# Optimization experiments

Measured on AMD Instinct MI355X. Metric: run time of the kernel, lower is better.

## Reference

```python
import jax, jax.numpy as jnp
import numpy as np

N, E = 50000, 800000
IN_DIM, HID, HEADS, OUT_DIM = 128, 64, 4, 40
NEG_SLOPE = 0.2


def setup_inputs() -> dict:
    key = jax.random.key(0)
    ks = jax.random.split(key, 12)
    x = jax.random.normal(ks[0], (N, IN_DIM), dtype=jnp.float32)
    edge_index = jax.random.randint(ks[1], (2, E), 0, N, dtype=jnp.int64)
    timesteps = jax.random.randint(ks[2], (N,), 0, 100, dtype=jnp.int64)
    s = 1.0 / np.sqrt(IN_DIM)
    W_proj = jax.random.uniform(ks[3], (IN_DIM, HID), jnp.float32, -s, s)
    b_proj = jnp.zeros((HID,), jnp.float32)
    time_emb = jax.random.normal(ks[4], (100, HID), dtype=jnp.float32)
    sg = 1.0 / np.sqrt(HID)
    W_gat = jax.random.uniform(ks[5], (HID, HEADS * HID), jnp.float32, -sg, sg)
    att_src = jax.random.uniform(ks[6], (HEADS, HID), jnp.float32, -sg, sg)
    att_dst = jax.random.uniform(ks[7], (HEADS, HID), jnp.float32, -sg, sg)
    b_gat = jnp.zeros((HEADS * HID,), jnp.float32)
    sc = 1.0 / np.sqrt(HEADS * HID)
    W_cls = jax.random.uniform(ks[8], (HEADS * HID, OUT_DIM), jnp.float32, -sc, sc)
    b_cls = jnp.zeros((OUT_DIM,), jnp.float32)
    return {"x": x, "edge_index": edge_index, "timesteps": timesteps,
            "W_proj": W_proj, "b_proj": b_proj, "time_emb": time_emb,
            "W_gat": W_gat, "att_src": att_src, "att_dst": att_dst, "b_gat": b_gat,
            "W_cls": W_cls, "b_cls": b_cls}


def reference(x, edge_index, timesteps, W_proj, b_proj, time_emb,
              W_gat, att_src, att_dst, b_gat, W_cls, b_cls):
    n = x.shape[0]
    # feature projection + ReLU + time embedding
    h0 = jax.nn.relu(x @ W_proj + b_proj) + time_emb[timesteps]  # [N, HID]
    # --- GATConv (PyG semantics, add_self_loops=True, concat heads) ---
    h = (h0 @ W_gat).reshape(n, HEADS, HID)              # [N, H, C]
    a_src = jnp.einsum('nhc,hc->nh', h, att_src)         # [N, H]
    a_dst = jnp.einsum('nhc,hc->nh', h, att_dst)
    loops = jnp.arange(n, dtype=edge_index.dtype)
    src = jnp.concatenate([edge_index[0], loops])        # [E+N]
    dst = jnp.concatenate([edge_index[1], loops])
    e = jax.nn.leaky_relu(a_src[src] + a_dst[dst], NEG_SLOPE)  # [E+N, H]
    # segment softmax over incoming edges per destination node
    m = jax.ops.segment_max(e, dst, num_segments=n)      # [N, H]
    p = jnp.exp(e - m[dst])
    denom = jax.ops.segment_sum(p, dst, num_segments=n)  # [N, H]
    alpha = p / (denom[dst] + 1e-16)                     # [E+N, H]
    msg = alpha[:, :, None] * h[src]                     # [E+N, H, C]
    agg = jax.ops.segment_sum(msg, dst, num_segments=n)  # [N, H, C]
    gat_out = agg.reshape(n, HEADS * HID) + b_gat
    # ReLU + (dropout is identity in eval) + classifier
    return jax.nn.relu(gat_out) @ W_cls + b_cls          # [N, OUT_DIM]
```

## Files before the change

kernel.cpp:

```cpp
#include <hip/hip_runtime.h>
#include <hip/hip_fp16.h>

#define IN_DIM 128
#define HID 64
#define HEADS 4
#define OUT_DIM 40
#define CAP 64
#define NEG 0.2f
#define PA_EPB 4096
#define BKT_SH 9
#define BKT_CAP 10240
#define GPAD 264

__device__ __forceinline__ float lrelu(float v) { return v > 0.f ? v : NEG * v; }

union HU { float2 f2; __half2 h2[2]; };
union HU2 { float4 f4; __half2 h2[4]; };

typedef _Float16 h2v __attribute__((ext_vector_type(2)));
union DU { float4 f4; h2v h[4]; };

typedef _Float16 f16x8 __attribute__((ext_vector_type(8)));
typedef float f32x4 __attribute__((ext_vector_type(4)));
union FU { float4 f4; f16x8 v; };

__device__ __forceinline__ float4 unpack_h4(float2 bits) {
    HU u; u.f2 = bits;
    float2 lo = __half22float2(u.h2[0]);
    float2 hi = __half22float2(u.h2[1]);
    return make_float4(lo.x, lo.y, hi.x, hi.y);
}

__global__ __launch_bounds__(256) void partA_kernel(
    const int* __restrict__ ei, int E, int nbkt, int paBlocks,
    int* __restrict__ cnt, unsigned int* __restrict__ ebuf,
    const float* __restrict__ Wg, const float* __restrict__ attS,
    const float* __restrict__ attD, const float* __restrict__ Wc,
    float* __restrict__ aSf, float* __restrict__ aDf,
    __half* __restrict__ WgT, __half* __restrict__ WcTg)
{
    if (blockIdx.x >= paBlocks) {
        int gid = (blockIdx.x - paBlocks) * 256 + threadIdx.x;
        if (gid < 256) {
            int k = gid >> 2, hd = gid & 3;
            const float* wr = Wg + k * 256 + hd * 64;
            const float* as = attS + hd * 64;
            const float* ad = attD + hd * 64;
            float ss = 0.f, dd = 0.f;
            for (int c = 0; c < 64; ++c) { float w = wr[c]; ss += w * as[c]; dd += w * ad[c]; }
            aSf[k * 4 + hd] = ss;
            aDf[k * 4 + hd] = dd;
        } else if (gid < 256 + 256 * HID) {
            int i = gid - 256;
            int o = i >> 6, k = i & 63;
            WgT[i] = __float2half(Wg[k * 256 + o]);
        } else if (gid < 256 + 256 * HID + OUT_DIM * 256) {
            int i = gid - 256 - 256 * HID;
            int o = i >> 8, k = i & 255;
            WcTg[i] = __float2half(Wc[k * OUT_DIM + o]);
        }
        return;
    }

    __shared__ int localCnt[128];
    __shared__ int baseArr[128];
    for (int i = threadIdx.x; i < nbkt; i += 256) localCnt[i] = 0;
    __syncthreads();

    const int e0 = blockIdx.x * PA_EPB + threadIdx.x;
    unsigned short l[16];
#pragma unroll
    for (int j = 0; j < 16; ++j) {
        int e = e0 + j * 256;
        if (e < E) {
            int d = ei[E + e];
            l[j] = (unsigned short)atomicAdd(&localCnt[d >> BKT_SH], 1);
        }
    }
    __syncthreads();
    for (int i = threadIdx.x; i < nbkt; i += 256)
        baseArr[i] = atomicAdd(&cnt[i], localCnt[i]);
    __syncthreads();
#pragma unroll
    for (int j = 0; j < 16; ++j) {
        int e = e0 + j * 256;
        if (e < E) {
            int s = ei[e];
            int d = ei[E + e];
            int b = d >> BKT_SH;
            int off = baseArr[b] + (int)l[j];
            if (off < BKT_CAP)
                ebuf[(size_t)b * BKT_CAP + off] =
                    ((unsigned)(d & ((1 << BKT_SH) - 1)) << 16) | (unsigned)s;
        }
    }
}

__global__ __launch_bounds__(256) void partB_kernel(
    const unsigned int* __restrict__ ebuf, const int* __restrict__ cnt,
    int* __restrict__ deg, unsigned short* __restrict__ csr, int N)
{
    __shared__ int cntL[512];
    __shared__ unsigned short rows[512 * CAP];
    const int b = blockIdx.x;
    for (int i = threadIdx.x; i < 512; i += 256) cntL[i] = 0;
    __syncthreads();

    int cb = cnt[b]; cb = cb < BKT_CAP ? cb : BKT_CAP;
    const unsigned int* eb = ebuf + (size_t)b * BKT_CAP;
    for (int i = threadIdx.x; i < cb; i += 256) {
        unsigned v = eb[i];
        int dloc = v >> 16;
        int slot = atomicAdd(&cntL[dloc], 1);
        if (slot < CAP) rows[dloc * CAP + slot] = (unsigned short)(v & 0xFFFFu);
    }
    __syncthreads();

    const int d0 = b << BKT_SH;
    for (int i = threadIdx.x; i < 512; i += 256) {
        int d = d0 + i;
        if (d < N) deg[d] = cntL[i];
    }
    int limRows = N - d0; limRows = limRows < 512 ? limRows : 512;
    if (limRows <= 0) return;
    const uint4* rsrc = (const uint4*)rows;
    uint4* rdst = (uint4*)(csr + (size_t)d0 * CAP);
    int nvec = (limRows * CAP) >> 3;
    for (int i = threadIdx.x; i < nvec; i += 256)
        rdst[i] = rsrc[i];
}

__global__ __launch_bounds__(256) void proj_kernel(
    const float* __restrict__ x, const float* __restrict__ Wp,
    const float* __restrict__ bp, const float* __restrict__ temb,
    const int* __restrict__ ts, const float* __restrict__ aSf,
    const float* __restrict__ aDf,
    __half* __restrict__ h0h, float* __restrict__ aS, float* __restrict__ aD, int N)
{
    __shared__ __half Wl[IN_DIM * HID];
    for (int i = threadIdx.x * 8; i < IN_DIM * HID; i += 256 * 8) {
        float4 wa = *(const float4*)(Wp + i);
        float4 wb = *(const float4*)(Wp + i + 4);
        HU2 u;
        u.h2[0] = __floats2half2_rn(wa.x, wa.y);
        u.h2[1] = __floats2half2_rn(wa.z, wa.w);
        u.h2[2] = __floats2half2_rn(wb.x, wb.y);
        u.h2[3] = __floats2half2_rn(wb.z, wb.w);
        *(float4*)(Wl + i) = u.f4;
    }
    __syncthreads();

    const int t = threadIdx.x;
    const int lane = t & 63, wq = t >> 6;
    const int cg = lane & 15, ng = lane >> 4;
    const int c0 = cg * 4;
    const int nodeBase = blockIdx.x * 32 + wq * 8 + ng * 2;

    float4 acc[2];
#pragma unroll
    for (int j = 0; j < 2; ++j) acc[j] = make_float4(0.f, 0.f, 0.f, 0.f);

    for (int k0 = 0; k0 < IN_DIM; k0 += 4) {
        float4 xv[2];
#pragma unroll
        for (int j = 0; j < 2; ++j) {
            int n = nodeBase + j; n = n < N ? n : N - 1;
            xv[j] = *(const float4*)(x + (size_t)n * IN_DIM + k0);
        }
        float4 wv[4];
#pragma unroll
        for (int kk = 0; kk < 4; ++kk)
            wv[kk] = unpack_h4(*(const float2*)(Wl + (k0 + kk) * HID + c0));
#pragma unroll
        for (int j = 0; j < 2; ++j) {
            const float* xs = (const float*)&xv[j];
#pragma unroll
            for (int kk = 0; kk < 4; ++kk) {
                acc[j].x += xs[kk] * wv[kk].x;
                acc[j].y += xs[kk] * wv[kk].y;
                acc[j].z += xs[kk] * wv[kk].z;
                acc[j].w += xs[kk] * wv[kk].w;
            }
        }
    }
    const float4 bb = *(const float4*)(bp + c0);
    float4 s0 = *(const float4*)(aSf + (c0 + 0) * 4);
    float4 s1 = *(const float4*)(aSf + (c0 + 1) * 4);
    float4 s2 = *(const float4*)(aSf + (c0 + 2) * 4);
    float4 s3 = *(const float4*)(aSf + (c0 + 3) * 4);
    float4 d0 = *(const float4*)(aDf + (c0 + 0) * 4);
    float4 d1 = *(const float4*)(aDf + (c0 + 1) * 4);
    float4 d2 = *(const float4*)(aDf + (c0 + 2) * 4);
    float4 d3 = *(const float4*)(aDf + (c0 + 3) * 4);
#pragma unroll
    for (int j = 0; j < 2; ++j) {
        int n = nodeBase + j;
        float4 r = make_float4(0.f, 0.f, 0.f, 0.f);
        if (n < N) {
            int tv = ts[n];
            float4 te = *(const float4*)(temb + (size_t)tv * HID + c0);
            r.x = fmaxf(acc[j].x + bb.x, 0.f) + te.x;
            r.y = fmaxf(acc[j].y + bb.y, 0.f) + te.y;
            r.z = fmaxf(acc[j].z + bb.z, 0.f) + te.z;
            r.w = fmaxf(acc[j].w + bb.w, 0.f) + te.w;
            HU u;
            u.h2[0] = __floats2half2_rn(r.x, r.y);
            u.h2[1] = __floats2half2_rn(r.z, r.w);
            *(float2*)(h0h + (size_t)n * HID + c0) = u.f2;
        }
        float4 pS, pD;
        pS.x = r.x * s0.x + r.y * s1.x + r.z * s2.x + r.w * s3.x;
        pS.y = r.x * s0.y + r.y * s1.y + r.z * s2.y + r.w * s3.y;
        pS.z = r.x * s0.z + r.y * s1.z + r.z * s2.z + r.w * s3.z;
        pS.w = r.x * s0.w + r.y * s1.w + r.z * s2.w + r.w * s3.w;
        pD.x = r.x * d0.x + r.y * d1.x + r.z * d2.x + r.w * d3.x;
        pD.y = r.x * d0.y + r.y * d1.y + r.z * d2.y + r.w * d3.y;
        pD.z = r.x * d0.z + r.y * d1.z + r.z * d2.z + r.w * d3.z;
        pD.w = r.x * d0.w + r.y * d1.w + r.z * d2.w + r.w * d3.w;
#pragma unroll
        for (int off = 8; off > 0; off >>= 1) {
            pS.x += __shfl_down(pS.x, off); pS.y += __shfl_down(pS.y, off);
            pS.z += __shfl_down(pS.z, off); pS.w += __shfl_down(pS.w, off);
            pD.x += __shfl_down(pD.x, off); pD.y += __shfl_down(pD.y, off);
            pD.z += __shfl_down(pD.z, off); pD.w += __shfl_down(pD.w, off);
        }
        if (cg == 0 && n < N) {
            *(float4*)(aS + (size_t)n * 4) = pS;
            *(float4*)(aD + (size_t)n * 4) = pD;
        }
    }
}

__global__ __launch_bounds__(256) void agg_kernel(
    const __half* __restrict__ h0h, const float* __restrict__ aS,
    const float* __restrict__ aD, const int* __restrict__ deg,
    const unsigned short* __restrict__ csr, __half* __restrict__ agg0h, int N)
{
    __shared__ float p_lds[4 * CAP * HEADS];
    __shared__ int   s_lds[4 * CAP];

    const int t = threadIdx.x;
    const int lane = t & 63, wq = t >> 6;
    const int n = blockIdx.x * 4 + wq;
    if (n >= N) return;
    const int hd16 = lane >> 4, li = lane & 15;

    const float adn = aD[n * 4 + hd16];
    const float es = lrelu(aS[n * 4 + hd16] + adn);

    int dn = deg[n]; dn = dn < CAP ? dn : CAP;
    const unsigned short* cs = csr + (size_t)n * CAP;
    float* pL = p_lds + wq * CAP * HEADS;
    int*   sL = s_lds + wq * CAP;

    float m = -1e30f;
    for (int i = li; i < dn; i += 16) {
        int src = cs[i];
        if (hd16 == 0) sL[i] = src << 7;
        float e = lrelu(aS[src * 4 + hd16] + adn);
        pL[i * HEADS + hd16] = e;
        m = fmaxf(m, e);
    }
#pragma unroll
    for (int off = 8; off > 0; off >>= 1)
        m = fmaxf(m, __shfl_xor(m, off));
    m = fmaxf(m, es);
    float mh[4], esh[4];
#pragma unroll
    for (int h = 0; h < 4; ++h) {
        mh[h]  = __shfl(m, h * 16);
        esh[h] = __shfl(es, h * 16);
    }

    float sp = 0.f;
    for (int idx = lane; idx < dn * 4; idx += 64) {
        float p = __expf(pL[idx] - mh[idx & 3]);
        pL[idx] = p;
        sp += p;
    }
#pragma unroll
    for (int off = 4; off < 64; off <<= 1)
        sp += __shfl_xor(sp, off);
    float pselfh[4], invh[4];
#pragma unroll
    for (int h = 0; h < 4; ++h) {
        float sh = __shfl(sp, h);
        pselfh[h] = __expf(esh[h] - mh[h]);
        invh[h] = 1.f / (sh + pselfh[h] + 1e-16f);
    }

    const int half = lane >> 5;
    const int ch2 = lane & 31;
    const char* hb = (const char*)h0h;
    const int laneByte = ch2 << 2;

    float2 acc[4];
    {
        float lo = 0.f, hi = 0.f;
        if (half == 0) {
            __half2 v2 = *(const __half2*)(hb + ((size_t)n << 7) + laneByte);
            float2 f = __half22float2(v2);
            lo = f.x; hi = f.y;
        }
#pragma unroll
        for (int h = 0; h < 4; ++h) {
            acc[h].x = pselfh[h] * lo;
            acc[h].y = pselfh[h] * hi;
        }
    }
    int i = 0;
    for (; i + 8 <= dn; i += 8) {
        int off0 = sL[i + 0 + half];
        int off1 = sL[i + 2 + half];
        int off2 = sL[i + 4 + half];
        int off3 = sL[i + 6 + half];
        __half2 v0 = *(const __half2*)(hb + off0 + laneByte);
        __half2 v1 = *(const __half2*)(hb + off1 + laneByte);
        __half2 v2 = *(const __half2*)(hb + off2 + laneByte);
        __half2 v3 = *(const __half2*)(hb + off3 + laneByte);
        float4 p0 = *(const float4*)(pL + (i + 0 + half) * 4);
        float4 p1 = *(const float4*)(pL + (i + 2 + half) * 4);
        float4 p2 = *(const float4*)(pL + (i + 4 + half) * 4);
        float4 p3 = *(const float4*)(pL + (i + 6 + half) * 4);
        float2 f;
        f = __half22float2(v0);
        acc[0].x += p0.x * f.x; acc[0].y += p0.x * f.y;
        acc[1].x += p0.y * f.x; acc[1].y += p0.y * f.y;
        acc[2].x += p0.z * f.x; acc[2].y += p0.z * f.y;
        acc[3].x += p0.w * f.x; acc[3].y += p0.w * f.y;
        f = __half22float2(v1);
        acc[0].x += p1.x * f.x; acc[0].y += p1.x * f.y;
        acc[1].x += p1.y * f.x; acc[1].y += p1.y * f.y;
        acc[2].x += p1.z * f.x; acc[2].y += p1.z * f.y;
        acc[3].x += p1.w * f.x; acc[3].y += p1.w * f.y;
        f = __half22float2(v2);
        acc[0].x += p2.x * f.x; acc[0].y += p2.x * f.y;
        acc[1].x += p2.y * f.x; acc[1].y += p2.y * f.y;
        acc[2].x += p2.z * f.x; acc[2].y += p2.z * f.y;
        acc[3].x += p2.w * f.x; acc[3].y += p2.w * f.y;
        f = __half22float2(v3);
        acc[0].x += p3.x * f.x; acc[0].y += p3.x * f.y;
        acc[1].x += p3.y * f.x; acc[1].y += p3.y * f.y;
        acc[2].x += p3.z * f.x; acc[2].y += p3.z * f.y;
        acc[3].x += p3.w * f.x; acc[3].y += p3.w * f.y;
    }
    for (; i + 2 <= dn; i += 2) {
        int off0 = sL[i + half];
        __half2 v0 = *(const __half2*)(hb + off0 + laneByte);
        float4 p0 = *(const float4*)(pL + (i + half) * 4);
        float2 f = __half22float2(v0);
        acc[0].x += p0.x * f.x; acc[0].y += p0.x * f.y;
        acc[1].x += p0.y * f.x; acc[1].y += p0.y * f.y;
        acc[2].x += p0.z * f.x; acc[2].y += p0.z * f.y;
        acc[3].x += p0.w * f.x; acc[3].y += p0.w * f.y;
    }
    if (i < dn && half == 0) {
        int off0 = sL[i];
        __half2 v0 = *(const __half2*)(hb + off0 + laneByte);
        float4 p0 = *(const float4*)(pL + i * 4);
        float2 f = __half22float2(v0);
        acc[0].x += p0.x * f.x; acc[0].y += p0.x * f.y;
        acc[1].x += p0.y * f.x; acc[1].y += p0.y * f.y;
        acc[2].x += p0.z * f.x; acc[2].y += p0.z * f.y;
        acc[3].x += p0.w * f.x; acc[3].y += p0.w * f.y;
    }
#pragma unroll
    for (int h = 0; h < 4; ++h) {
        acc[h].x += __shfl_xor(acc[h].x, 32);
        acc[h].y += __shfl_xor(acc[h].y, 32);
    }
    if (lane < 32) {
        __half2* dst = (__half2*)(agg0h + (size_t)n * 256);
#pragma unroll
        for (int h = 0; h < 4; ++h)
            dst[h * 32 + ch2] = __floats2half2_rn(acc[h].x * invh[h],
                                                  acc[h].y * invh[h]);
    }
}

__global__ __launch_bounds__(256) void gatcls_kernel(
    const __half* __restrict__ agg0h, const __half* __restrict__ WgT,
    const float* __restrict__ bg, const __half* __restrict__ WcTg,
    const float* __restrict__ bc, float* __restrict__ out, int N)
{
    __shared__ __half gtile[32 * GPAD];

    const int t = threadIdx.x;
    const int lane = t & 63, wq = t >> 6;
    const int m16 = lane & 15, quad = lane >> 4;
    const int nodeBase = blockIdx.x * 32;

    {
        const int h = wq;
        f32x4 acc[2][4];
#pragma unroll
        for (int mt = 0; mt < 2; ++mt)
#pragma unroll
            for (int nt = 0; nt < 4; ++nt)
                acc[mt][nt] = (f32x4){0.f, 0.f, 0.f, 0.f};

#pragma unroll
        for (int ks = 0; ks < 2; ++ks) {
            FU a[2], b[4];
#pragma unroll
            for (int mt = 0; mt < 2; ++mt) {
                int n = nodeBase + mt * 16 + m16; n = n < N ? n : N - 1;
                a[mt].f4 = *(const float4*)(agg0h + (size_t)n * 256 + h * 64 + ks * 32 + quad * 8);
            }
#pragma unroll
            for (int nt = 0; nt < 4; ++nt) {
                int o = h * 64 + nt * 16 + m16;
                b[nt].f4 = *(const float4*)(WgT + o * 64 + ks * 32 + quad * 8);
            }
#pragma unroll
            for (int mt = 0; mt < 2; ++mt)
#pragma unroll
                for (int nt = 0; nt < 4; ++nt)
                    acc[mt][nt] = __builtin_amdgcn_mfma_f32_16x16x32_f16(
                        a[mt].v, b[nt].v, acc[mt][nt], 0, 0, 0);
        }
#pragma unroll
        for (int nt = 0; nt < 4; ++nt) {
            int o = h * 64 + nt * 16 + m16;
            float bv = bg[o];
#pragma unroll
            for (int mt = 0; mt < 2; ++mt) {
#pragma unroll
                for (int r = 0; r < 4; ++r) {
                    int nloc = mt * 16 + quad * 4 + r;
                    gtile[nloc * GPAD + o] = __float2half(fmaxf(acc[mt][nt][r] + bv, 0.f));
                }
            }
        }
    }
    __syncthreads();

    {
        const int mt = wq >> 1;
        const int ntCount = (wq & 1) ? 1 : 2;
        const int ntBase = (wq & 1) ? 2 : 0;
        f32x4 acc2[2];
        acc2[0] = (f32x4){0.f, 0.f, 0.f, 0.f};
        acc2[1] = (f32x4){0.f, 0.f, 0.f, 0.f};
#pragma unroll
        for (int ks = 0; ks < 8; ++ks) {
            FU a; a.f4 = *(const float4*)(gtile + (mt * 16 + m16) * GPAD + ks * 32 + quad * 8);
            for (int q = 0; q < ntCount; ++q) {
                int o = (ntBase + q) * 16 + m16;
                int oc = o < OUT_DIM ? o : OUT_DIM - 1;
                FU b; b.f4 = *(const float4*)(WcTg + oc * 256 + ks * 32 + quad * 8);
                acc2[q] = __builtin_amdgcn_mfma_f32_16x16x32_f16(a.v, b.v, acc2[q], 0, 0, 0);
            }
        }
        for (int q = 0; q < ntCount; ++q) {
            int o = (ntBase + q) * 16 + m16;
            if (o < OUT_DIM) {
                float bv = bc[o];
#pragma unroll
                for (int r = 0; r < 4; ++r) {
                    int n = nodeBase + mt * 16 + quad * 4 + r;
                    if (n < N) out[(size_t)n * OUT_DIM + o] = acc2[q][r] + bv;
                }
            }
        }
    }
}

extern "C" void kernel_launch(void* const* d_in, const int* in_sizes, int n_in,
                              void* d_out, int out_size, void* d_ws, size_t ws_size,
                              hipStream_t stream) {
    const float* x    = (const float*)d_in[0];
    const int*   ei   = (const int*)d_in[1];
    const int*   ts   = (const int*)d_in[2];
    const float* Wp   = (const float*)d_in[3];
    const float* bp   = (const float*)d_in[4];
    const float* temb = (const float*)d_in[5];
    const float* Wg   = (const float*)d_in[6];
    const float* attS = (const float*)d_in[7];
    const float* attD = (const float*)d_in[8];
    const float* bg   = (const float*)d_in[9];
    const float* Wc   = (const float*)d_in[10];
    const float* bc   = (const float*)d_in[11];
    float* out = (float*)d_out;

    const int N = in_sizes[0] / IN_DIM;
    const int E = in_sizes[1] / 2;
    const int nbkt = (N + (1 << BKT_SH) - 1) >> BKT_SH;

    char* w = (char*)d_ws;
    __half*         h0h   = (__half*)w;         w += (size_t)N * HID * 2;
    __half*         agg0h = (__half*)w;         w += (size_t)N * 256 * 2;
    float*          aS    = (float*)w;          w += (size_t)N * HEADS * 4;
    float*          aD    = (float*)w;          w += (size_t)N * HEADS * 4;
    int*            deg   = (int*)w;            w += (size_t)N * 4;
    unsigned short* csr   = (unsigned short*)w; w += (size_t)N * CAP * 2;
    unsigned int*   ebuf  = (unsigned int*)w;   w += (size_t)nbkt * BKT_CAP * 4;
    int*            cnt   = (int*)w;            w += (size_t)nbkt * 4;
    float*          aSf   = (float*)w;          w += 256 * 4;
    float*          aDf   = (float*)w;          w += 256 * 4;
    __half*         WgT   = (__half*)w;         w += (size_t)256 * HID * 2;
    __half*         WcTg  = (__half*)w;         w += (size_t)OUT_DIM * 256 * 2;

    const int paBlocks = (E + PA_EPB - 1) / PA_EPB;
    const int prepWork = 256 + 256 * HID + OUT_DIM * 256;
    const int prepBlocks = (prepWork + 255) / 256;

    hipMemsetAsync(cnt, 0, (size_t)nbkt * 4, stream);
    partA_kernel<<<paBlocks + prepBlocks, 256, 0, stream>>>(
        ei, E, nbkt, paBlocks, cnt, ebuf, Wg, attS, attD, Wc, aSf, aDf, WgT, WcTg);
    partB_kernel<<<nbkt, 256, 0, stream>>>(ebuf, cnt, deg, csr, N);
    proj_kernel<<<(N + 31) / 32, 256, 0, stream>>>(x, Wp, bp, temb, ts, aSf, aDf,
                                                   h0h, aS, aD, N);
    agg_kernel<<<(N + 3) / 4, 256, 0, stream>>>(h0h, aS, aD, deg, csr, agg0h, N);
    gatcls_kernel<<<(N + 31) / 32, 256, 0, stream>>>(agg0h, WgT, bg, WcTg, bc, out, N);
}
```

Baseline: 211.2 us.

## Use fp16 dot2 projection with pre-packed weights and smaller edge buckets

The projection kernel now converts x to half2 pairs and accumulates with fdot2 against a k-pair-packed fp16 weight table. That table is built once in the partA prep blocks, which removes the per-block shared-memory staging of Wp and its barrier. The edge bucketing is also halved (256-node buckets, 2048 edges per partition block), so partB uses half the LDS, gets more blocks and has better occupancy. The trade-off is extra fp16 rounding of the x inputs, and many more buckets feeding the global count atomics.

```diff
diff --git a/kernel.cpp b/kernel.cpp
--- a/kernel.cpp
+++ b/kernel.cpp
@@ -7,9 +7,9 @@
 #define OUT_DIM 40
 #define CAP 64
 #define NEG 0.2f
-#define PA_EPB 4096
-#define BKT_SH 9
-#define BKT_CAP 10240
+#define PA_EPB 2048
+#define BKT_SH 8
+#define BKT_CAP 5120
 #define GPAD 264
 
 __device__ __forceinline__ float lrelu(float v) { return v > 0.f ? v : NEG * v; }
@@ -19,6 +19,7 @@
 
 typedef _Float16 h2v __attribute__((ext_vector_type(2)));
 union DU { float4 f4; h2v h[4]; };
+union H2U { __half2 h2; h2v v; };
 
 typedef _Float16 f16x8 __attribute__((ext_vector_type(8)));
 typedef float f32x4 __attribute__((ext_vector_type(4)));
@@ -36,8 +37,10 @@
     int* __restrict__ cnt, unsigned int* __restrict__ ebuf,
     const float* __restrict__ Wg, const float* __restrict__ attS,
     const float* __restrict__ attD, const float* __restrict__ Wc,
+    const float* __restrict__ Wp,
     float* __restrict__ aSf, float* __restrict__ aDf,
-    __half* __restrict__ WgT, __half* __restrict__ WcTg)
+    __half* __restrict__ WgT, __half* __restrict__ WcTg,
+    __half2* __restrict__ Wpp)
 {
     if (blockIdx.x >= paBlocks) {
         int gid = (blockIdx.x - paBlocks) * 256 + threadIdx.x;
@@ -58,19 +61,23 @@
             int i = gid - 256 - 256 * HID;
             int o = i >> 8, k = i & 255;
             WcTg[i] = __float2half(Wc[k * OUT_DIM + o]);
+        } else if (gid < 256 + 256 * HID + OUT_DIM * 256 + 64 * 64) {
+            int i = gid - 256 - 256 * HID - OUT_DIM * 256;
+            int kp = i >> 6, c = i & 63;
+            Wpp[i] = __floats2half2_rn(Wp[(2 * kp) * HID + c], Wp[(2 * kp + 1) * HID + c]);
         }
         return;
     }
 
-    __shared__ int localCnt[128];
-    __shared__ int baseArr[128];
+    __shared__ int localCnt[256];
+    __shared__ int baseArr[256];
     for (int i = threadIdx.x; i < nbkt; i += 256) localCnt[i] = 0;
     __syncthreads();
 
     const int e0 = blockIdx.x * PA_EPB + threadIdx.x;
-    unsigned short l[16];
-#pragma unroll
-    for (int j = 0; j < 16; ++j) {
+    unsigned short l[8];
+#pragma unroll
+    for (int j = 0; j < 8; ++j) {
         int e = e0 + j * 256;
         if (e < E) {
             int d = ei[E + e];
@@ -82,7 +89,7 @@
         baseArr[i] = atomicAdd(&cnt[i], localCnt[i]);
     __syncthreads();
 #pragma unroll
-    for (int j = 0; j < 16; ++j) {
+    for (int j = 0; j < 8; ++j) {
         int e = e0 + j * 256;
         if (e < E) {
             int s = ei[e];
@@ -100,10 +107,10 @@
     const unsigned int* __restrict__ ebuf, const int* __restrict__ cnt,
     int* __restrict__ deg, unsigned short* __restrict__ csr, int N)
 {
-    __shared__ int cntL[512];
-    __shared__ unsigned short rows[512 * CAP];
+    __shared__ int cntL[256];
+    __shared__ unsigned short rows[256 * CAP];
     const int b = blockIdx.x;
-    for (int i = threadIdx.x; i < 512; i += 256) cntL[i] = 0;
+    for (int i = threadIdx.x; i < 256; i += 256) cntL[i] = 0;
     __syncthreads();
 
     int cb = cnt[b]; cb = cb < BKT_CAP ? cb : BKT_CAP;
@@ -117,11 +124,11 @@
     __syncthreads();
 
     const int d0 = b << BKT_SH;
-    for (int i = threadIdx.x; i < 512; i += 256) {
+    for (int i = threadIdx.x; i < 256; i += 256) {
         int d = d0 + i;
         if (d < N) deg[d] = cntL[i];
     }
-    int limRows = N - d0; limRows = limRows < 512 ? limRows : 512;
+    int limRows = N - d0; limRows = limRows < 256 ? limRows : 256;
     if (limRows <= 0) return;
     const uint4* rsrc = (const uint4*)rows;
     uint4* rdst = (uint4*)(csr + (size_t)d0 * CAP);
@@ -131,25 +138,12 @@
 }
 
 __global__ __launch_bounds__(256) void proj_kernel(
-    const float* __restrict__ x, const float* __restrict__ Wp,
+    const float* __restrict__ x, const __half2* __restrict__ Wpp,
     const float* __restrict__ bp, const float* __restrict__ temb,
     const int* __restrict__ ts, const float* __restrict__ aSf,
     const float* __restrict__ aDf,
     __half* __restrict__ h0h, float* __restrict__ aS, float* __restrict__ aD, int N)
 {
-    __shared__ __half Wl[IN_DIM * HID];
-    for (int i = threadIdx.x * 8; i < IN_DIM * HID; i += 256 * 8) {
-        float4 wa = *(const float4*)(Wp + i);
-        float4 wb = *(const float4*)(Wp + i + 4);
-        HU2 u;
-        u.h2[0] = __floats2half2_rn(wa.x, wa.y);
-        u.h2[1] = __floats2half2_rn(wa.z, wa.w);
-        u.h2[2] = __floats2half2_rn(wb.x, wb.y);
-        u.h2[3] = __floats2half2_rn(wb.z, wb.w);
-        *(float4*)(Wl + i) = u.f4;
-    }
-    __syncthreads();
-
     const int t = threadIdx.x;
     const int lane = t & 63, wq = t >> 6;
     const int cg = lane & 15, ng = lane >> 4;
@@ -160,26 +154,28 @@
 #pragma unroll
     for (int j = 0; j < 2; ++j) acc[j] = make_float4(0.f, 0.f, 0.f, 0.f);
 
-    for (int k0 = 0; k0 < IN_DIM; k0 += 4) {
-        float4 xv[2];
+    for (int k0 = 0; k0 < IN_DIM; k0 += 8) {
+        H2U xp[2][4];
 #pragma unroll
         for (int j = 0; j < 2; ++j) {
             int n = nodeBase + j; n = n < N ? n : N - 1;
-            xv[j] = *(const float4*)(x + (size_t)n * IN_DIM + k0);
-        }
-        float4 wv[4];
-#pragma unroll
-        for (int kk = 0; kk < 4; ++kk)
-            wv[kk] = unpack_h4(*(const float2*)(Wl + (k0 + kk) * HID + c0));
-#pragma unroll
-        for (int j = 0; j < 2; ++j) {
-            const float* xs = (const float*)&xv[j];
-#pragma unroll
-            for (int kk = 0; kk < 4; ++kk) {
-                acc[j].x += xs[kk] * wv[kk].x;
-                acc[j].y += xs[kk] * wv[kk].y;
-                acc[j].z += xs[kk] * wv[kk].z;
-                acc[j].w += xs[kk] * wv[kk].w;
+            float4 xa = *(const float4*)(x + (size_t)n * IN_DIM + k0);
+            float4 xb = *(const float4*)(x + (size_t)n * IN_DIM + k0 + 4);
+            xp[j][0].h2 = __floats2half2_rn(xa.x, xa.y);
+            xp[j][1].h2 = __floats2half2_rn(xa.z, xa.w);
+            xp[j][2].h2 = __floats2half2_rn(xb.x, xb.y);
+            xp[j][3].h2 = __floats2half2_rn(xb.z, xb.w);
+        }
+        const int kp0 = k0 >> 1;
+#pragma unroll
+        for (int p = 0; p < 4; ++p) {
+            DU wv; wv.f4 = *(const float4*)(Wpp + (kp0 + p) * HID + c0);
+#pragma unroll
+            for (int j = 0; j < 2; ++j) {
+                acc[j].x = __builtin_amdgcn_fdot2(xp[j][p].v, wv.h[0], acc[j].x, false);
+                acc[j].y = __builtin_amdgcn_fdot2(xp[j][p].v, wv.h[1], acc[j].y, false);
+                acc[j].z = __builtin_amdgcn_fdot2(xp[j][p].v, wv.h[2], acc[j].z, false);
+                acc[j].w = __builtin_amdgcn_fdot2(xp[j][p].v, wv.h[3], acc[j].w, false);
             }
         }
     }
@@ -500,16 +496,18 @@
     float*          aDf   = (float*)w;          w += 256 * 4;
     __half*         WgT   = (__half*)w;         w += (size_t)256 * HID * 2;
     __half*         WcTg  = (__half*)w;         w += (size_t)OUT_DIM * 256 * 2;
+    __half2*        Wpp   = (__half2*)w;        w += (size_t)64 * HID * 4;
 
     const int paBlocks = (E + PA_EPB - 1) / PA_EPB;
-    const int prepWork = 256 + 256 * HID + OUT_DIM * 256;
+    const int prepWork = 256 + 256 * HID + OUT_DIM * 256 + 64 * 64;
     const int prepBlocks = (prepWork + 255) / 256;
 
     hipMemsetAsync(cnt, 0, (size_t)nbkt * 4, stream);
     partA_kernel<<<paBlocks + prepBlocks, 256, 0, stream>>>(
-        ei, E, nbkt, paBlocks, cnt, ebuf, Wg, attS, attD, Wc, aSf, aDf, WgT, WcTg);
+        ei, E, nbkt, paBlocks, cnt, ebuf, Wg, attS, attD, Wc, Wp,
+        aSf, aDf, WgT, WcTg, Wpp);
     partB_kernel<<<nbkt, 256, 0, stream>>>(ebuf, cnt, deg, csr, N);
-    proj_kernel<<<(N + 31) / 32, 256, 0, stream>>>(x, Wp, bp, temb, ts, aSf, aDf,
+    proj_kernel<<<(N + 31) / 32, 256, 0, stream>>>(x, Wpp, bp, temb, ts, aSf, aDf,
                                                    h0h, aS, aD, N);
     agg_kernel<<<(N + 3) / 4, 256, 0, stream>>>(h0h, aS, aD, deg, csr, agg0h, N);
     gatcls_kernel<<<(N + 31) / 32, 256, 0, stream>>>(agg0h, WgT, bg, WcTg, bc, out, N);
```

Measured after the change: 213.0 us. Within noise of the previous version (+0.9%).
